# Kernel optimization log

Hardware: AMD Instinct MI355X
Metric: run time of the kernel (lower is better)

The kernel has to match this reference:

```python
import jax, jax.numpy as jnp
import numpy as np

B, H, W, C = 8, 128, 128, 256
WS, SS, NH = 8, 4, 8          # window size, shift size, num heads
HD = C // NH                   # head dim = 32
N = WS * WS                    # tokens per window = 64
NW = (H // WS) * (W // WS)     # windows per image = 256


def _rel_pos_index():
    coords = np.stack(np.meshgrid(np.arange(WS), np.arange(WS), indexing='ij'))  # (2,WS,WS)
    cf = coords.reshape(2, -1)
    rc = (cf[:, :, None] - cf[:, None, :]).transpose(1, 2, 0)
    rc[:, :, 0] += WS - 1
    rc[:, :, 1] += WS - 1
    rc[:, :, 0] *= 2 * WS - 1
    return rc.sum(-1)  # (N, N) int


def _attn_mask():
    # shift mask for SW-MSA, built from static shapes (matches torch img_mask construction)
    img = np.zeros((1, H, W, 1))
    sl = (slice(0, -WS), slice(-WS, -SS), slice(-SS, None))
    cnt = 0
    for h in sl:
        for w in sl:
            img[:, h, w, :] = cnt
            cnt += 1
    mw = img.reshape(1, H // WS, WS, W // WS, WS, 1).transpose(0, 1, 3, 2, 4, 5).reshape(-1, N)
    am = mw[:, None, :] - mw[:, :, None]  # (NW, N, N)
    return np.where(am != 0, -100.0, 0.0).astype(np.float32)


RPI = jnp.asarray(_rel_pos_index())      # (N, N)
AMASK = jnp.asarray(_attn_mask())        # (NW, N, N)


def _ln(x, g, b):
    m = x.mean(-1, keepdims=True)
    v = x.var(-1, keepdims=True)
    return (x - m) / jnp.sqrt(v + 1e-5) * g + b


def setup_inputs() -> dict:
    key = jax.random.key(0)
    ks = jax.random.split(key, 8)
    s = lambda k, shp, sc: jax.random.normal(k, shp, jnp.float32) * sc
    return {
        'x': s(ks[0], (B, H * W, C), 1.0),
        'norm1_g': jnp.ones((C,), jnp.float32), 'norm1_b': jnp.zeros((C,), jnp.float32),
        'qkv_w': s(ks[1], (3 * C, C), 0.02), 'qkv_b': jnp.zeros((3 * C,), jnp.float32),
        'rpb_table': s(ks[2], ((2 * WS - 1) ** 2, NH), 0.02),
        'proj_w': s(ks[3], (C, C), 0.02), 'proj_b': jnp.zeros((C,), jnp.float32),
        'norm2_g': jnp.ones((C,), jnp.float32), 'norm2_b': jnp.zeros((C,), jnp.float32),
        'fc1_w': s(ks[4], (4 * C, C), 0.02), 'fc1_b': jnp.zeros((4 * C,), jnp.float32),
        'fc2_w': s(ks[5], (C, 4 * C), 0.02), 'fc2_b': jnp.zeros((C,), jnp.float32),
    }


def reference(x, norm1_g, norm1_b, qkv_w, qkv_b, rpb_table, proj_w, proj_b,
              norm2_g, norm2_b, fc1_w, fc1_b, fc2_w, fc2_b):
    shortcut = x
    h = _ln(x, norm1_g, norm1_b).reshape(B, H, W, C)
    # cyclic shift
    h = jnp.roll(h, (-SS, -SS), axis=(1, 2))
    # window partition -> (B*NW, N, C)
    xw = h.reshape(B, H // WS, WS, W // WS, WS, C).transpose(0, 1, 3, 2, 4, 5).reshape(-1, N, C)
    qkv = (xw @ qkv_w.T + qkv_b).reshape(-1, N, 3, NH, HD).transpose(2, 0, 3, 1, 4)
    q, k, v = qkv[0], qkv[1], qkv[2]           # (B*NW, NH, N, HD)
    attn = jnp.einsum('bhnd,bhmd->bhnm', q * (float(HD) ** -0.5), k)
    bias = rpb_table[RPI.reshape(-1)].reshape(N, N, NH).transpose(2, 0, 1)  # (NH, N, N)
    attn = attn + bias[None]
    attn = attn.reshape(B, NW, NH, N, N) + AMASK[None, :, None]
    attn = jax.nn.softmax(attn.reshape(-1, NH, N, N), axis=-1)
    xw = jnp.einsum('bhnm,bhmd->bnhd', attn, v).reshape(-1, N, C)
    xw = xw @ proj_w.T + proj_b
    # window reverse + reverse shift
    h = xw.reshape(B, H // WS, W // WS, WS, WS, C).transpose(0, 1, 3, 2, 4, 5).reshape(B, H, W, C)
    h = jnp.roll(h, (SS, SS), axis=(1, 2)).reshape(B, H * W, C)
    x = shortcut + h
    # MLP block
    m = _ln(x, norm2_g, norm2_b)
    m = jax.nn.gelu(m @ fc1_w.T + fc1_b, approximate=False) @ fc2_w.T + fc2_b
    return x + m
```

## Files before the change

### kernel.cpp

```cpp
#include <hip/hip_runtime.h>
#include <hip/hip_bf16.h>
#include <math.h>

#define B_   8
#define H_   128
#define W_   128
#define C_   256
#define WS_  8
#define SS_  4
#define NH_  8
#define HD_  32
#define MROWS 131072

typedef short bf16x8 __attribute__((ext_vector_type(8)));
typedef float f32x4  __attribute__((ext_vector_type(4)));

__device__ __forceinline__ unsigned short f2bf(float f) {
    unsigned int u = __float_as_uint(f);
    u += 0x7fffu + ((u >> 16) & 1u);
    return (unsigned short)(u >> 16);
}
__device__ __forceinline__ float bfl(unsigned int u) {
    return __uint_as_float(u << 16);
}
__device__ __forceinline__ float bfh(unsigned int u) {
    return __uint_as_float(u & 0xffff0000u);
}

__device__ __forceinline__ unsigned int pk2(float a, float b) {
    __hip_bfloat162 h = __float22bfloat162_rn(make_float2(a, b));
    unsigned int u;
    __builtin_memcpy(&u, &h, 4);
    return u;
}

__device__ __forceinline__ void gload16(const unsigned short* g, unsigned short* l) {
    __builtin_amdgcn_global_load_lds(
        (const __attribute__((address_space(1))) unsigned int*)(const void*)g,
        (__attribute__((address_space(3))) unsigned int*)(void*)l, 16, 0, 0);
}

__device__ __forceinline__ float fast_gelu2(float v) {
    return v * __builtin_amdgcn_rcpf(1.0f + __expf(-1.702f * v));
}

__global__ __launch_bounds__(256) void cvt4(const float* __restrict__ s,
                                            unsigned short* __restrict__ d, int n) {
    const int i = (blockIdx.x * 256 + threadIdx.x) * 4;
    if (i >= n) return;
    const float4 v = *(const float4*)(s + i);
    ushort4 o;
    o.x = f2bf(v.x); o.y = f2bf(v.y); o.z = f2bf(v.z); o.w = f2bf(v.w);
    *(ushort4*)(d + i) = o;
}

template<int N>
__global__ __launch_bounds__(256, 2) void ln1_qkv(const float* __restrict__ x,
                                                  const float* __restrict__ g1,
                                                  const float* __restrict__ b1n,
                                                  const unsigned short* __restrict__ W,
                                                  const float* __restrict__ bias,
                                                  unsigned short* __restrict__ Cout) {
    __shared__ unsigned short W_lds[2][64 * 256];

    const int t    = threadIdx.x;
    const int wave = t >> 6, lane = t & 63;
    const int fr   = lane & 15, h = lane >> 4;
    const int m0   = blockIdx.x * 128;
    constexpr int NT = N / 64;

    auto stage = [&](int b, int nt) {
        const unsigned short* Wt = W + (size_t)nt * 64 * 256;
#pragma unroll
        for (int q = 0; q < 8; ++q) {
            const int d    = q * 4096 + t * 16;
            const int row  = d >> 9;
            const int colb = (d & 511) ^ ((row & 7) << 4);
            gload16(Wt + (size_t)row * 256 + (colb >> 1),
                    &W_lds[b][(q * 4096 + wave * 1024) >> 1]);
        }
    };

    stage(0, 0);

    bf16x8 aw[2][8];
#pragma unroll
    for (int mi = 0; mi < 2; ++mi) {
        const int m    = m0 + wave * 32 + mi * 16 + fr;
        const int bimg = m >> 14;
        const int rem  = m & 16383;
        const int win  = rem >> 6;
        const int tok  = rem & 63;
        const int hp = (win >> 4) * 8 + (tok >> 3);
        const int wp = (win & 15) * 8 + (tok & 7);
        const int ho = (hp + SS_) & (H_ - 1);
        const int wo = (wp + SS_) & (W_ - 1);
        const float* xr = x + ((size_t)(bimg << 14) + ho * W_ + wo) * C_;

        float4 va[8], vb[8];
        float s = 0.0f, ss = 0.0f;
#pragma unroll
        for (int ks = 0; ks < 8; ++ks) {
            va[ks] = *(const float4*)&xr[ks * 32 + h * 8];
            vb[ks] = *(const float4*)&xr[ks * 32 + h * 8 + 4];
            s  += va[ks].x + va[ks].y + va[ks].z + va[ks].w
                + vb[ks].x + vb[ks].y + vb[ks].z + vb[ks].w;
            ss += va[ks].x*va[ks].x + va[ks].y*va[ks].y + va[ks].z*va[ks].z + va[ks].w*va[ks].w
                + vb[ks].x*vb[ks].x + vb[ks].y*vb[ks].y + vb[ks].z*vb[ks].z + vb[ks].w*vb[ks].w;
        }
        s  += __shfl_xor(s, 16, 64);  s  += __shfl_xor(s, 32, 64);
        ss += __shfl_xor(ss, 16, 64); ss += __shfl_xor(ss, 32, 64);
        const float mean = s * (1.0f / 256.0f);
        const float rstd = rsqrtf(ss * (1.0f / 256.0f) - mean * mean + 1e-5f);

#pragma unroll
        for (int ks = 0; ks < 8; ++ks) {
            const float4 g0 = *(const float4*)&g1 [ks * 32 + h * 8];
            const float4 g4 = *(const float4*)&g1 [ks * 32 + h * 8 + 4];
            const float4 c0 = *(const float4*)&b1n[ks * 32 + h * 8];
            const float4 c4 = *(const float4*)&b1n[ks * 32 + h * 8 + 4];
            uint4 u;
            u.x = pk2((va[ks].x - mean) * rstd * g0.x + c0.x,
                      (va[ks].y - mean) * rstd * g0.y + c0.y);
            u.y = pk2((va[ks].z - mean) * rstd * g0.z + c0.z,
                      (va[ks].w - mean) * rstd * g0.w + c0.w);
            u.z = pk2((vb[ks].x - mean) * rstd * g4.x + c4.x,
                      (vb[ks].y - mean) * rstd * g4.y + c4.y);
            u.w = pk2((vb[ks].z - mean) * rstd * g4.z + c4.z,
                      (vb[ks].w - mean) * rstd * g4.w + c4.w);
            aw[mi][ks] = *(bf16x8*)&u;
        }
    }

    __syncthreads();

    for (int nt = 0; nt < NT; ++nt) {
        if (nt + 1 < NT) stage((nt + 1) & 1, nt + 1);

        const char* buf = (const char*)W_lds[nt & 1];
        f32x4 acc[2][4] = {};
#pragma unroll
        for (int nj = 0; nj < 4; ++nj) {
            const int   wrow = nj * 16 + fr;
            const char* wb   = buf + wrow * 512;
            const int   swz  = (fr & 7) << 4;
            bf16x8 wf[8];
#pragma unroll
            for (int ks = 0; ks < 8; ++ks)
                wf[ks] = *(const bf16x8*)(wb + ((ks * 64 + h * 16) ^ swz));
#pragma unroll
            for (int ks = 0; ks < 8; ++ks) {
                acc[0][nj] = __builtin_amdgcn_mfma_f32_16x16x32_bf16(wf[ks], aw[0][ks], acc[0][nj], 0, 0, 0);
                acc[1][nj] = __builtin_amdgcn_mfma_f32_16x16x32_bf16(wf[ks], aw[1][ks], acc[1][nj], 0, 0, 0);
            }
        }

#pragma unroll
        for (int nj = 0; nj < 4; ++nj) {
            const int n = nt * 64 + nj * 16 + h * 4;
            const float4 bb = *(const float4*)&bias[n];
#pragma unroll
            for (int mi = 0; mi < 2; ++mi) {
                const int m = m0 + wave * 32 + mi * 16 + fr;
                uint2 pk;
                pk.x = pk2(acc[mi][nj][0] + bb.x, acc[mi][nj][1] + bb.y);
                pk.y = pk2(acc[mi][nj][2] + bb.z, acc[mi][nj][3] + bb.w);
                *(uint2*)&Cout[(size_t)m * N + n] = pk;
            }
        }
        __syncthreads();
    }
}

__global__ __launch_bounds__(512, 2) void mlp_fused(const unsigned short* __restrict__ A,
                                                    const unsigned short* __restrict__ W1,
                                                    const float* __restrict__ b1,
                                                    const unsigned short* __restrict__ W2,
                                                    const float* __restrict__ b2,
                                                    const unsigned short* __restrict__ x1b,
                                                    float* __restrict__ out) {
    __shared__ unsigned short W1_lds[2][32 * 256];
    __shared__ unsigned short W2_lds[2][256 * 32];
    __shared__ unsigned short G_lds [2][256 * 32];

    const int t    = threadIdx.x;
    const int wave = t >> 6, lane = t & 63;
    const int fr   = lane & 15, h = lane >> 4;
    const int wr   = wave >> 2, wc = wave & 3;
    const int m0   = blockIdx.x * 256;
    constexpr int NC = 32;

    bf16x8 aw[2][8];
    const unsigned short* Abase = A + (size_t)(m0 + wave * 32 + fr) * 256 + h * 8;
#pragma unroll
    for (int mi = 0; mi < 2; ++mi)
#pragma unroll
        for (int ks = 0; ks < 8; ++ks)
            aw[mi][ks] = *(const bf16x8*)(Abase + mi * 16 * 256 + ks * 32);

    auto stageW1 = [&](int b, int c) {
        const unsigned short* Wt = W1 + (size_t)c * 32 * 256;
#pragma unroll
        for (int q = 0; q < 2; ++q) {
            const int d    = q * 8192 + t * 16;
            const int row  = d >> 9;
            const int colb = (d & 511) ^ ((row & 7) << 4);
            gload16(Wt + (size_t)row * 256 + (colb >> 1),
                    &W1_lds[b][(q * 8192 + wave * 1024) >> 1]);
        }
    };
    auto stageW2 = [&](int b, int c) {
#pragma unroll
        for (int q = 0; q < 2; ++q) {
            const int d    = q * 8192 + t * 16;
            const int row  = d >> 6;
            const int colb = (d & 63) ^ ((row & 3) << 4);
            gload16(W2 + (size_t)row * 1024 + c * 32 + (colb >> 1),
                    &W2_lds[b][(q * 8192 + wave * 1024) >> 1]);
        }
    };

    auto fc1 = [&](int cc, int gb) {
        const char* buf = (const char*)W1_lds[cc & 1];
        const int   swz = (fr & 7) << 4;
#pragma unroll
        for (int nj = 0; nj < 2; ++nj) {
            const int   wrow = nj * 16 + fr;
            const char* wb   = buf + wrow * 512;
            bf16x8 wf[8];
#pragma unroll
            for (int ks = 0; ks < 8; ++ks)
                wf[ks] = *(const bf16x8*)(wb + ((ks * 64 + h * 16) ^ swz));
            f32x4 g0 = {}, g1 = {};
#pragma unroll
            for (int ks = 0; ks < 8; ++ks) {
                g0 = __builtin_amdgcn_mfma_f32_16x16x32_bf16(wf[ks], aw[0][ks], g0, 0, 0, 0);
                g1 = __builtin_amdgcn_mfma_f32_16x16x32_bf16(wf[ks], aw[1][ks], g1, 0, 0, 0);
            }
            const float4 bb = *(const float4*)&b1[cc * 32 + nj * 16 + h * 4];
            {
                const int row = wave * 32 + fr;
                const int off = (nj * 32 + h * 8) ^ ((row & 3) << 4);
                uint2 pk;
                pk.x = pk2(fast_gelu2(g0[0] + bb.x), fast_gelu2(g0[1] + bb.y));
                pk.y = pk2(fast_gelu2(g0[2] + bb.z), fast_gelu2(g0[3] + bb.w));
                *(uint2*)((char*)G_lds[gb] + row * 64 + off) = pk;
            }
            {
                const int row = wave * 32 + 16 + fr;
                const int off = (nj * 32 + h * 8) ^ ((row & 3) << 4);
                uint2 pk;
                pk.x = pk2(fast_gelu2(g1[0] + bb.x), fast_gelu2(g1[1] + bb.y));
                pk.y = pk2(fast_gelu2(g1[2] + bb.z), fast_gelu2(g1[3] + bb.w));
                *(uint2*)((char*)G_lds[gb] + row * 64 + off) = pk;
            }
        }
    };

    f32x4 acc2[8][4] = {};

    stageW1(0, 0);
    stageW2(0, 0);
    asm volatile("s_waitcnt vmcnt(0)" ::: "memory");
    __builtin_amdgcn_sched_barrier(0);
    __builtin_amdgcn_s_barrier();
    stageW1(1, 1);
    fc1(0, 0);

    for (int c = 0; c < NC; ++c) {
        asm volatile("s_waitcnt vmcnt(0) lgkmcnt(0)" ::: "memory");
        __builtin_amdgcn_sched_barrier(0);
        __builtin_amdgcn_s_barrier();

        if (c + 2 < NC) stageW1(c & 1, c + 2);
        if (c + 1 < NC) stageW2((c + 1) & 1, c + 1);

        {
            const char* Gb = (const char*)G_lds[c & 1];
            const char* Wb = (const char*)W2_lds[c & 1];
            bf16x8 gf[8];
#pragma unroll
            for (int mi2 = 0; mi2 < 8; ++mi2) {
                const int grow = wr * 128 + mi2 * 16 + fr;
                gf[mi2] = *(const bf16x8*)(Gb + grow * 64 + ((h * 16) ^ ((grow & 3) << 4)));
            }
#pragma unroll
            for (int nj2 = 0; nj2 < 4; ++nj2) {
                const int wrow2 = wc * 64 + nj2 * 16 + fr;
                const bf16x8 w2f = *(const bf16x8*)(Wb + wrow2 * 64 + ((h * 16) ^ ((wrow2 & 3) << 4)));
#pragma unroll
                for (int mi2 = 0; mi2 < 8; ++mi2)
                    acc2[mi2][nj2] = __builtin_amdgcn_mfma_f32_16x16x32_bf16(
                        w2f, gf[mi2], acc2[mi2][nj2], 0, 0, 0);
            }
        }

        if (c + 1 < NC) fc1(c + 1, (c + 1) & 1);
    }

    float4 bv[4];
#pragma unroll
    for (int nj2 = 0; nj2 < 4; ++nj2)
        bv[nj2] = *(const float4*)&b2[wc * 64 + nj2 * 16 + h * 4];

#pragma unroll
    for (int mi2 = 0; mi2 < 8; ++mi2) {
        const int m = m0 + wr * 128 + mi2 * 16 + fr;
#pragma unroll
        for (int nj2 = 0; nj2 < 4; ++nj2) {
            const int n = wc * 64 + nj2 * 16 + h * 4;
            const size_t idx = (size_t)m * 256 + n;
            const uint2 rb = *(const uint2*)&x1b[idx];
            float4 o;
            o.x = acc2[mi2][nj2][0] + bv[nj2].x + bfl(rb.x);
            o.y = acc2[mi2][nj2][1] + bv[nj2].y + bfh(rb.x);
            o.z = acc2[mi2][nj2][2] + bv[nj2].z + bfl(rb.y);
            o.w = acc2[mi2][nj2][3] + bv[nj2].w + bfh(rb.y);
            *(float4*)&out[idx] = o;
        }
    }
}

__global__ __launch_bounds__(256, 2) void proj_ln2(const unsigned short* __restrict__ A,
                                                   const unsigned short* __restrict__ W,
                                                   const float* __restrict__ bias,
                                                   const float* __restrict__ resid,
                                                   const float* __restrict__ g2,
                                                   const float* __restrict__ b2,
                                                   unsigned short* __restrict__ x1b,
                                                   unsigned short* __restrict__ ln2out) {
    __shared__ unsigned short W_lds[2][64 * 256];

    const int t    = threadIdx.x;
    const int wave = t >> 6, lane = t & 63;
    const int fr   = lane & 15, h = lane >> 4;
    const int m0   = blockIdx.x * 128;

    bf16x8 aw[2][8];
    const unsigned short* Abase = A + (size_t)(m0 + wave * 32 + fr) * 256 + h * 8;
#pragma unroll
    for (int mi = 0; mi < 2; ++mi)
#pragma unroll
        for (int ks = 0; ks < 8; ++ks)
            aw[mi][ks] = *(const bf16x8*)(Abase + mi * 16 * 256 + ks * 32);

    auto stage = [&](int b, int nt) {
        const unsigned short* Wt = W + (size_t)nt * 64 * 256;
#pragma unroll
        for (int q = 0; q < 8; ++q) {
            const int d    = q * 4096 + t * 16;
            const int row  = d >> 9;
            const int colb = (d & 511) ^ ((row & 7) << 4);
            gload16(Wt + (size_t)row * 256 + (colb >> 1),
                    &W_lds[b][(q * 4096 + wave * 1024) >> 1]);
        }
    };

    stage(0, 0);
    __syncthreads();

    f32x4 acc[2][16] = {};
    for (int nt = 0; nt < 4; ++nt) {
        if (nt < 3) stage((nt + 1) & 1, nt + 1);
        const char* buf = (const char*)W_lds[nt & 1];
#pragma unroll
        for (int nj = 0; nj < 4; ++nj) {
            const int   wrow = nj * 16 + fr;
            const char* wb   = buf + wrow * 512;
            const int   swz  = (fr & 7) << 4;
            bf16x8 wf[8];
#pragma unroll
            for (int ks = 0; ks < 8; ++ks)
                wf[ks] = *(const bf16x8*)(wb + ((ks * 64 + h * 16) ^ swz));
            switch (nt) {
            case 0:
#pragma unroll
                for (int ks = 0; ks < 8; ++ks) {
                    acc[0][0 + nj] = __builtin_amdgcn_mfma_f32_16x16x32_bf16(wf[ks], aw[0][ks], acc[0][0 + nj], 0, 0, 0);
                    acc[1][0 + nj] = __builtin_amdgcn_mfma_f32_16x16x32_bf16(wf[ks], aw[1][ks], acc[1][0 + nj], 0, 0, 0);
                } break;
            case 1:
#pragma unroll
                for (int ks = 0; ks < 8; ++ks) {
                    acc[0][4 + nj] = __builtin_amdgcn_mfma_f32_16x16x32_bf16(wf[ks], aw[0][ks], acc[0][4 + nj], 0, 0, 0);
                    acc[1][4 + nj] = __builtin_amdgcn_mfma_f32_16x16x32_bf16(wf[ks], aw[1][ks], acc[1][4 + nj], 0, 0, 0);
                } break;
            case 2:
#pragma unroll
                for (int ks = 0; ks < 8; ++ks) {
                    acc[0][8 + nj] = __builtin_amdgcn_mfma_f32_16x16x32_bf16(wf[ks], aw[0][ks], acc[0][8 + nj], 0, 0, 0);
                    acc[1][8 + nj] = __builtin_amdgcn_mfma_f32_16x16x32_bf16(wf[ks], aw[1][ks], acc[1][8 + nj], 0, 0, 0);
                } break;
            default:
#pragma unroll
                for (int ks = 0; ks < 8; ++ks) {
                    acc[0][12 + nj] = __builtin_amdgcn_mfma_f32_16x16x32_bf16(wf[ks], aw[0][ks], acc[0][12 + nj], 0, 0, 0);
                    acc[1][12 + nj] = __builtin_amdgcn_mfma_f32_16x16x32_bf16(wf[ks], aw[1][ks], acc[1][12 + nj], 0, 0, 0);
                } break;
            }
        }
        __syncthreads();
    }

#pragma unroll
    for (int mi = 0; mi < 2; ++mi) {
        const int m    = m0 + wave * 32 + mi * 16 + fr;
        const int bimg = m >> 14;
        const int rem  = m & 16383;
        const int win  = rem >> 6;
        const int tok  = rem & 63;
        const int hp = (win >> 4) * 8 + (tok >> 3);
        const int wp = (win & 15) * 8 + (tok & 7);
        const int ho = (hp + SS_) & (H_ - 1);
        const int wo = (wp + SS_) & (W_ - 1);
        const size_t drow = ((size_t)(bimg << 14) + ho * W_ + wo) * 256;

        float sum = 0.0f, ssum = 0.0f;
#pragma unroll
        for (int u = 0; u < 16; ++u) {
            const int n = (u >> 2) * 64 + (u & 3) * 16 + h * 4;
            const float4 bb = *(const float4*)&bias[n];
            const float4 r4 = *(const float4*)&resid[drow + n];
            float4 v;
            v.x = acc[mi][u][0] + bb.x + r4.x;
            v.y = acc[mi][u][1] + bb.y + r4.y;
            v.z = acc[mi][u][2] + bb.z + r4.z;
            v.w = acc[mi][u][3] + bb.w + r4.w;
            uint2 pk;
            pk.x = pk2(v.x, v.y);
            pk.y = pk2(v.z, v.w);
            *(uint2*)&x1b[drow + n] = pk;
            sum  += v.x + v.y + v.z + v.w;
            ssum += v.x*v.x + v.y*v.y + v.z*v.z + v.w*v.w;
        }
        sum  += __shfl_xor(sum, 16, 64);  sum  += __shfl_xor(sum, 32, 64);
        ssum += __shfl_xor(ssum, 16, 64); ssum += __shfl_xor(ssum, 32, 64);
        const float mean = sum * (1.0f / 256.0f);
        const float rstd = rsqrtf(ssum * (1.0f / 256.0f) - mean * mean + 1e-5f);

#pragma unroll
        for (int u = 0; u < 16; ++u) {
            const int n = (u >> 2) * 64 + (u & 3) * 16 + h * 4;
            const uint2 rb = *(const uint2*)&x1b[drow + n];
            const float4 gg = *(const float4*)&g2[n];
            const float4 bb = *(const float4*)&b2[n];
            uint2 pk;
            pk.x = pk2((bfl(rb.x) - mean) * rstd * gg.x + bb.x,
                       (bfh(rb.x) - mean) * rstd * gg.y + bb.y);
            pk.y = pk2((bfl(rb.y) - mean) * rstd * gg.z + bb.z,
                       (bfh(rb.y) - mean) * rstd * gg.w + bb.w);
            *(uint2*)&ln2out[drow + n] = pk;
        }
    }
}

__device__ __forceinline__ int grp_(int p) { return p < (H_ - WS_) ? 0 : (p < (H_ - SS_) ? 1 : 2); }

__global__ __launch_bounds__(256) void attn_kernel(const unsigned short* __restrict__ qkv,
                                                   const float* __restrict__ rpb,
                                                   unsigned short* __restrict__ out) {
    __shared__ unsigned short P [4][64 * 72];
    __shared__ unsigned short Vt[4][32 * 72];
    __shared__ float rpb_s[232];

    const int t    = threadIdx.x;
    const int wid  = t >> 6, lane = t & 63;
    const int head = blockIdx.x & 7;
    const int win  = (blockIdx.x >> 3) * 4 + wid;
    const int fr   = lane & 15, h = lane >> 4;

    if (t < 225) rpb_s[t] = rpb[t * 8 + head];
    __syncthreads();

    const size_t qbase = (size_t)win * 64 * 768 + head * HD_;

    bf16x8 ak[4], bq[4];
#pragma unroll
    for (int ki = 0; ki < 4; ++ki)
        ak[ki] = *(const bf16x8*)&qkv[qbase + (size_t)(ki * 16 + fr) * 768 + 256 + h * 8];
#pragma unroll
    for (int qj = 0; qj < 4; ++qj)
        bq[qj] = *(const bf16x8*)&qkv[qbase + (size_t)(qj * 16 + fr) * 768 + h * 8];

    {
        const unsigned short* vrow = &qkv[qbase + (size_t)lane * 768 + 512];
#pragma unroll
        for (int dv = 0; dv < 32; dv += 8) {
            bf16x8 v8 = *(const bf16x8*)&vrow[dv];
#pragma unroll
            for (int j = 0; j < 8; ++j)
                Vt[wid][(dv + j) * 72 + lane] = ((unsigned short*)&v8)[j];
        }
    }

    f32x4 st[4][4] = {};
#pragma unroll
    for (int ki = 0; ki < 4; ++ki)
#pragma unroll
        for (int qj = 0; qj < 4; ++qj)
            st[ki][qj] = __builtin_amdgcn_mfma_f32_16x16x32_bf16(ak[ki], bq[qj], st[ki][qj], 0, 0, 0);

    const int wim = win & 255;
    const int whb = (wim >> 4) * 8, wwb = (wim & 15) * 8;
    const float qscale = 0.17677669529663687f;

#pragma unroll
    for (int qj = 0; qj < 4; ++qj) {
        const int q  = qj * 16 + fr;
        const int yq = q >> 3, xq = q & 7;
        const int gq = grp_(whb + yq) * 3 + grp_(wwb + xq);
        float s[16];
#pragma unroll
        for (int ki = 0; ki < 4; ++ki)
#pragma unroll
            for (int r = 0; r < 4; ++r) {
                const int k  = ki * 16 + h * 4 + r;
                const int yk = k >> 3, xk = k & 7;
                const int gk = grp_(whb + yk) * 3 + grp_(wwb + xk);
                float v = fmaf(st[ki][qj][r], qscale,
                               rpb_s[(yq - yk + 7) * 15 + (xq - xk + 7)]);
                if (gk != gq) v -= 100.0f;
                s[ki * 4 + r] = v;
            }
        float m = s[0];
#pragma unroll
        for (int i = 1; i < 16; ++i) m = fmaxf(m, s[i]);
        m = fmaxf(m, __shfl_xor(m, 16, 64));
        m = fmaxf(m, __shfl_xor(m, 32, 64));
        float sum = 0.0f;
#pragma unroll
        for (int i = 0; i < 16; ++i) { s[i] = __expf(s[i] - m); sum += s[i]; }
        sum += __shfl_xor(sum, 16, 64);
        sum += __shfl_xor(sum, 32, 64);
        const float rinv = __builtin_amdgcn_rcpf(sum);
#pragma unroll
        for (int ki = 0; ki < 4; ++ki)
#pragma unroll
            for (int rp = 0; rp < 4; rp += 2) {
                const unsigned int lo = f2bf(s[ki * 4 + rp]     * rinv);
                const unsigned int hi = f2bf(s[ki * 4 + rp + 1] * rinv);
                *(unsigned int*)&P[wid][q * 72 + ki * 16 + h * 4 + rp] = lo | (hi << 16);
            }
    }

    f32x4 oacc[4][2] = {};
#pragma unroll
    for (int ks = 0; ks < 2; ++ks) {
        bf16x8 pa[4], vb[2];
#pragma unroll
        for (int qi = 0; qi < 4; ++qi)
            pa[qi] = *(const bf16x8*)&P[wid][(qi * 16 + fr) * 72 + ks * 32 + h * 8];
#pragma unroll
        for (int nj = 0; nj < 2; ++nj)
            vb[nj] = *(const bf16x8*)&Vt[wid][(nj * 16 + fr) * 72 + ks * 32 + h * 8];
#pragma unroll
        for (int qi = 0; qi < 4; ++qi)
#pragma unroll
            for (int nj = 0; nj < 2; ++nj)
                oacc[qi][nj] = __builtin_amdgcn_mfma_f32_16x16x32_bf16(pa[qi], vb[nj], oacc[qi][nj], 0, 0, 0);
    }

#pragma unroll
    for (int qi = 0; qi < 4; ++qi)
#pragma unroll
        for (int nj = 0; nj < 2; ++nj)
#pragma unroll
            for (int r = 0; r < 4; ++r) {
                const int q = qi * 16 + h * 4 + r;
                const int d = nj * 16 + fr;
                out[((size_t)win * 64 + q) * C_ + head * HD_ + d] = f2bf(oacc[qi][nj][r]);
            }
}

extern "C" void kernel_launch(void* const* d_in, const int* in_sizes, int n_in,
                              void* d_out, int out_size, void* d_ws, size_t ws_size,
                              hipStream_t stream) {
    const float* x      = (const float*)d_in[0];
    const float* n1g    = (const float*)d_in[1];
    const float* n1b    = (const float*)d_in[2];
    const float* qkv_w  = (const float*)d_in[3];
    const float* qkv_b  = (const float*)d_in[4];
    const float* rpb    = (const float*)d_in[5];
    const float* proj_w = (const float*)d_in[6];
    const float* proj_b = (const float*)d_in[7];
    const float* n2g    = (const float*)d_in[8];
    const float* n2b    = (const float*)d_in[9];
    const float* fc1_w  = (const float*)d_in[10];
    const float* fc1_b  = (const float*)d_in[11];
    const float* fc2_w  = (const float*)d_in[12];
    const float* fc2_b  = (const float*)d_in[13];
    float* out = (float*)d_out;

    unsigned short* wq  = (unsigned short*)d_ws;
    unsigned short* rA  = wq + (1u << 20);
    unsigned short* rB  = rA + 33554432u;
    unsigned short* rB2 = rB + 100663296u;
    unsigned short* x1b = rB;

    unsigned short* qkv_wb  = wq;
    unsigned short* proj_wb = wq + 196608;
    unsigned short* fc1_wb  = wq + 262144;
    unsigned short* fc2_wb  = wq + 524288;

    cvt4<<<192, 256, 0, stream>>>(qkv_w,  qkv_wb,  196608);
    cvt4<<<64,  256, 0, stream>>>(proj_w, proj_wb, 65536);
    cvt4<<<256, 256, 0, stream>>>(fc1_w,  fc1_wb,  262144);
    cvt4<<<256, 256, 0, stream>>>(fc2_w,  fc2_wb,  262144);

    ln1_qkv<768><<<MROWS / 128, 256, 0, stream>>>(x, n1g, n1b, qkv_wb, qkv_b, rB);
    attn_kernel<<<(2048 / 4) * NH_, 256, 0, stream>>>(rB, rpb, rB2);
    proj_ln2<<<MROWS / 128, 256, 0, stream>>>(rB2, proj_wb, proj_b, x, n2g, n2b, x1b, rA);
    mlp_fused<<<MROWS / 256, 512, 0, stream>>>(rA, fc1_wb, fc1_b, fc2_wb, fc2_b, x1b, out);
}
```

Before: 554.3 us.

## Double mlp_fused block to 1024 threads, halving per-wave rows and accumulators

The fused MLP kernel now runs 16 waves per block instead of 8. Each wave handles 16 rows in fc1 and a 64x64 fc2 sub-tile, so the A-fragment registers and fc2 accumulators are halved and each thread issues one staging load instead of two. The fc2 loop order is swapped so W2 fragments are held in registers and G fragments are streamed. This trades fewer registers and more parallel waves per block for more waves sharing each barrier and only one 1024-thread block per CU.

```diff
diff --git a/kernel.cpp b/kernel.cpp
--- a/kernel.cpp
+++ b/kernel.cpp
@@ -172,13 +172,13 @@
     }
 }
 
-__global__ __launch_bounds__(512, 2) void mlp_fused(const unsigned short* __restrict__ A,
-                                                    const unsigned short* __restrict__ W1,
-                                                    const float* __restrict__ b1,
-                                                    const unsigned short* __restrict__ W2,
-                                                    const float* __restrict__ b2,
-                                                    const unsigned short* __restrict__ x1b,
-                                                    float* __restrict__ out) {
+__global__ __launch_bounds__(1024) void mlp_fused(const unsigned short* __restrict__ A,
+                                                  const unsigned short* __restrict__ W1,
+                                                  const float* __restrict__ b1,
+                                                  const unsigned short* __restrict__ W2,
+                                                  const float* __restrict__ b2,
+                                                  const unsigned short* __restrict__ x1b,
+                                                  float* __restrict__ out) {
     __shared__ unsigned short W1_lds[2][32 * 256];
     __shared__ unsigned short W2_lds[2][256 * 32];
     __shared__ unsigned short G_lds [2][256 * 32];
@@ -190,34 +190,26 @@
     const int m0   = blockIdx.x * 256;
     constexpr int NC = 32;
 
-    bf16x8 aw[2][8];
-    const unsigned short* Abase = A + (size_t)(m0 + wave * 32 + fr) * 256 + h * 8;
-#pragma unroll
-    for (int mi = 0; mi < 2; ++mi)
-#pragma unroll
-        for (int ks = 0; ks < 8; ++ks)
-            aw[mi][ks] = *(const bf16x8*)(Abase + mi * 16 * 256 + ks * 32);
+    bf16x8 aw[8];
+    const unsigned short* Abase = A + (size_t)(m0 + wave * 16 + fr) * 256 + h * 8;
+#pragma unroll
+    for (int ks = 0; ks < 8; ++ks)
+        aw[ks] = *(const bf16x8*)(Abase + ks * 32);
 
     auto stageW1 = [&](int b, int c) {
         const unsigned short* Wt = W1 + (size_t)c * 32 * 256;
-#pragma unroll
-        for (int q = 0; q < 2; ++q) {
-            const int d    = q * 8192 + t * 16;
-            const int row  = d >> 9;
-            const int colb = (d & 511) ^ ((row & 7) << 4);
-            gload16(Wt + (size_t)row * 256 + (colb >> 1),
-                    &W1_lds[b][(q * 8192 + wave * 1024) >> 1]);
-        }
+        const int d    = t * 16;
+        const int row  = d >> 9;
+        const int colb = (d & 511) ^ ((row & 7) << 4);
+        gload16(Wt + (size_t)row * 256 + (colb >> 1),
+                &W1_lds[b][(wave * 1024) >> 1]);
     };
     auto stageW2 = [&](int b, int c) {
-#pragma unroll
-        for (int q = 0; q < 2; ++q) {
-            const int d    = q * 8192 + t * 16;
-            const int row  = d >> 6;
-            const int colb = (d & 63) ^ ((row & 3) << 4);
-            gload16(W2 + (size_t)row * 1024 + c * 32 + (colb >> 1),
-                    &W2_lds[b][(q * 8192 + wave * 1024) >> 1]);
-        }
+        const int d    = t * 16;
+        const int row  = d >> 6;
+        const int colb = (d & 63) ^ ((row & 3) << 4);
+        gload16(W2 + (size_t)row * 1024 + c * 32 + (colb >> 1),
+                &W2_lds[b][(wave * 1024) >> 1]);
     };
 
     auto fc1 = [&](int cc, int gb) {
@@ -227,37 +219,28 @@
         for (int nj = 0; nj < 2; ++nj) {
             const int   wrow = nj * 16 + fr;
             const char* wb   = buf + wrow * 512;
-            bf16x8 wf[8];
-#pragma unroll
-            for (int ks = 0; ks < 8; ++ks)
-                wf[ks] = *(const bf16x8*)(wb + ((ks * 64 + h * 16) ^ swz));
-            f32x4 g0 = {}, g1 = {};
-#pragma unroll
-            for (int ks = 0; ks < 8; ++ks) {
-                g0 = __builtin_amdgcn_mfma_f32_16x16x32_bf16(wf[ks], aw[0][ks], g0, 0, 0, 0);
-                g1 = __builtin_amdgcn_mfma_f32_16x16x32_bf16(wf[ks], aw[1][ks], g1, 0, 0, 0);
+            f32x4 g0 = {};
+#pragma unroll
+            for (int kh = 0; kh < 2; ++kh) {
+                bf16x8 wf[4];
+#pragma unroll
+                for (int ks = 0; ks < 4; ++ks)
+                    wf[ks] = *(const bf16x8*)(wb + (((kh * 4 + ks) * 64 + h * 16) ^ swz));
+#pragma unroll
+                for (int ks = 0; ks < 4; ++ks)
+                    g0 = __builtin_amdgcn_mfma_f32_16x16x32_bf16(wf[ks], aw[kh * 4 + ks], g0, 0, 0, 0);
             }
             const float4 bb = *(const float4*)&b1[cc * 32 + nj * 16 + h * 4];
-            {
-                const int row = wave * 32 + fr;
-                const int off = (nj * 32 + h * 8) ^ ((row & 3) << 4);
-                uint2 pk;
-                pk.x = pk2(fast_gelu2(g0[0] + bb.x), fast_gelu2(g0[1] + bb.y));
-                pk.y = pk2(fast_gelu2(g0[2] + bb.z), fast_gelu2(g0[3] + bb.w));
-                *(uint2*)((char*)G_lds[gb] + row * 64 + off) = pk;
-            }
-            {
-                const int row = wave * 32 + 16 + fr;
-                const int off = (nj * 32 + h * 8) ^ ((row & 3) << 4);
-                uint2 pk;
-                pk.x = pk2(fast_gelu2(g1[0] + bb.x), fast_gelu2(g1[1] + bb.y));
-                pk.y = pk2(fast_gelu2(g1[2] + bb.z), fast_gelu2(g1[3] + bb.w));
-                *(uint2*)((char*)G_lds[gb] + row * 64 + off) = pk;
-            }
+            const int row = wave * 16 + fr;
+            const int off = (nj * 32 + h * 8) ^ ((row & 3) << 4);
+            uint2 pk;
+            pk.x = pk2(fast_gelu2(g0[0] + bb.x), fast_gelu2(g0[1] + bb.y));
+            pk.y = pk2(fast_gelu2(g0[2] + bb.z), fast_gelu2(g0[3] + bb.w));
+            *(uint2*)((char*)G_lds[gb] + row * 64 + off) = pk;
         }
     };
 
-    f32x4 acc2[8][4] = {};
+    f32x4 acc2[4][4] = {};
 
     stageW1(0, 0);
     stageW2(0, 0);
@@ -278,20 +261,20 @@
         {
             const char* Gb = (const char*)G_lds[c & 1];
             const char* Wb = (const char*)W2_lds[c & 1];
-            bf16x8 gf[8];
-#pragma unroll
-            for (int mi2 = 0; mi2 < 8; ++mi2) {
-                const int grow = wr * 128 + mi2 * 16 + fr;
-                gf[mi2] = *(const bf16x8*)(Gb + grow * 64 + ((h * 16) ^ ((grow & 3) << 4)));
-            }
+            bf16x8 w2f[4];
 #pragma unroll
             for (int nj2 = 0; nj2 < 4; ++nj2) {
                 const int wrow2 = wc * 64 + nj2 * 16 + fr;
-                const bf16x8 w2f = *(const bf16x8*)(Wb + wrow2 * 64 + ((h * 16) ^ ((wrow2 & 3) << 4)));
-#pragma unroll
-                for (int mi2 = 0; mi2 < 8; ++mi2)
+                w2f[nj2] = *(const bf16x8*)(Wb + wrow2 * 64 + ((h * 16) ^ ((wrow2 & 3) << 4)));
+            }
+#pragma unroll
+            for (int mi2 = 0; mi2 < 4; ++mi2) {
+                const int grow = wr * 64 + mi2 * 16 + fr;
+                const bf16x8 gf = *(const bf16x8*)(Gb + grow * 64 + ((h * 16) ^ ((grow & 3) << 4)));
+#pragma unroll
+                for (int nj2 = 0; nj2 < 4; ++nj2)
                     acc2[mi2][nj2] = __builtin_amdgcn_mfma_f32_16x16x32_bf16(
-                        w2f, gf[mi2], acc2[mi2][nj2], 0, 0, 0);
+                        w2f[nj2], gf, acc2[mi2][nj2], 0, 0, 0);
             }
         }
 
@@ -304,8 +287,8 @@
         bv[nj2] = *(const float4*)&b2[wc * 64 + nj2 * 16 + h * 4];
 
 #pragma unroll
-    for (int mi2 = 0; mi2 < 8; ++mi2) {
-        const int m = m0 + wr * 128 + mi2 * 16 + fr;
+    for (int mi2 = 0; mi2 < 4; ++mi2) {
+        const int m = m0 + wr * 64 + mi2 * 16 + fr;
 #pragma unroll
         for (int nj2 = 0; nj2 < 4; ++nj2) {
             const int n = wc * 64 + nj2 * 16 + h * 4;
@@ -610,5 +593,5 @@
     ln1_qkv<768><<<MROWS / 128, 256, 0, stream>>>(x, n1g, n1b, qkv_wb, qkv_b, rB);
     attn_kernel<<<(2048 / 4) * NH_, 256, 0, stream>>>(rB, rpb, rB2);
     proj_ln2<<<MROWS / 128, 256, 0, stream>>>(rB2, proj_wb, proj_b, x, n2g, n2b, x1b, rA);
-    mlp_fused<<<MROWS / 256, 512, 0, stream>>>(rA, fc1_wb, fc1_b, fc2_wb, fc2_b, x1b, out);
-}
+    mlp_fused<<<MROWS / 256, 1024, 0, stream>>>(rA, fc1_wb, fc1_b, fc2_wb, fc2_b, x1b, out);
+}
```

Result: slower. 597.5 us (+7.8%).
